# Optimization experiments

Hardware: AMD Instinct MI355X
Metric: run time of the kernel (lower is better)

## Reference

```python
import jax, jax.numpy as jnp
import numpy as np

N, F, H, R, B, L, C, E, NB = 8192, 512, 256, 16, 32, 256, 7, 262144, 30
D = F + H


def setup_inputs() -> dict:
    ks = jax.random.split(jax.random.key(0), 16)
    g = lambda k, shape, fan: jax.random.normal(k, shape, jnp.float32) / np.sqrt(fan)
    return {
        "x": jax.random.normal(ks[0], (N, F), jnp.float32),
        "edge_index": jax.random.randint(ks[1], (2, E), 0, N),
        "edge_norm": jax.random.uniform(ks[2], (E,), jnp.float32),
        "edge_type": jax.random.randint(ks[3], (E,), 0, R),
        "seq_lengths": jnp.full((B,), L, dtype=jnp.int32),
        "umask": jnp.ones((B, L), jnp.float32),
        "nodal_attn": 1,
        "avec": 0,
        "basis": g(ks[4], (NB, F, H), F),
        "comp": g(ks[5], (R, NB), NB),
        "root1": g(ks[6], (F, H), F),
        "bias1": jnp.zeros((H,), jnp.float32),
        "w_rel": g(ks[7], (H, H), H),
        "b_rel": jnp.zeros((H,), jnp.float32),
        "w_root": g(ks[8], (H, H), H),
        "w_att": g(ks[9], (D, D), D),
        "b_att": jnp.zeros((D,), jnp.float32),
        "w_lin": g(ks[10], (D, H), D),
        "b_lin": jnp.zeros((H,), jnp.float32),
        "w_fc": g(ks[11], (H, C), H),
        "b_fc": jnp.zeros((C,), jnp.float32),
    }


def reference(x, edge_index, edge_norm, edge_type, seq_lengths, umask,
              nodal_attn, avec, basis, comp, root1, bias1, w_rel, b_rel,
              w_root, w_att, b_att, w_lin, b_lin, w_fc, b_fc):
    n = x.shape[0]
    r = comp.shape[0]
    src, dst = edge_index[0], edge_index[1]
    # ---- RGCNConv (num_bases basis decomposition, mean aggregation per relation, root + bias)
    W = jnp.einsum('rb,bfh->rfh', comp, basis)             # [R,F,H]
    xw = jnp.einsum('nf,rfh->nrh', x, W)                   # [N,R,H]
    msg = xw[src, edge_type]                               # [E,H] gather per edge
    seg = dst * r + edge_type                              # per (node, relation) segment
    cnt = jax.ops.segment_sum(jnp.ones((msg.shape[0],), msg.dtype), seg, num_segments=n * r)
    msg = msg / jnp.maximum(cnt[seg], 1.0)[:, None]
    out1 = jax.ops.segment_sum(msg, dst, num_segments=n) + x @ root1 + bias1
    # ---- GraphConv (add aggregation): W_rel * sum_j h_j + b_rel + W_root * h_i
    agg2 = jax.ops.segment_sum(out1[src], dst, num_segments=n)
    out2 = agg2 @ w_rel + b_rel + out1 @ w_root
    emotions = jnp.concatenate([x, out2], axis=-1)          # [N, F+H]
    if int(nodal_attn):
        seq = np.asarray(seq_lengths)                       # static conversation lengths
        starts = np.concatenate([[0], np.cumsum(seq)[:-1]])
        lmax = int(seq.max())
        rows = [jnp.pad(jax.lax.dynamic_slice_in_dim(emotions, int(s), int(l)),
                        ((0, lmax - int(l)), (0, 0)))
                for s, l in zip(starts, seq)]
        M = jnp.stack(rows, 0).transpose(1, 0, 2)           # [L, B, D]
        mask = umask                                        # [B, L]
        # MatchingAttention 'general2', vectorized over all timesteps t
        X = M @ w_att + b_att                               # transform(x_t) for every t: [L,B,D]
        Mm = M * mask.T[:, :, None]                         # mask memory over seq dim
        scores = jnp.einsum('tbd,sbd->tbs', X, Mm) * mask[None]
        a = jax.nn.softmax(jnp.tanh(scores), axis=-1) * mask[None]
        a = a / jnp.sum(a, axis=-1, keepdims=True)
        att = jnp.einsum('tbs,sbd->tbd', a, M)              # [L,B,D]
        hidden = jax.nn.relu(att @ w_lin + b_lin)
    else:
        hidden = jax.nn.relu(emotions @ w_lin + b_lin)
    # dropout is identity in eval mode
    logits = hidden @ w_fc + b_fc
    if int(avec):
        return logits
    return jax.nn.log_softmax(logits, axis=1)  # faithful: torch uses dim=1
```

## Files before the change

### kernel.cpp

```cpp
#include <hip/hip_runtime.h>
#include <hip/hip_bf16.h>

#define NN 8192
#define FF 512
#define HH 256
#define RR 16
#define BB 32
#define LL 256
#define CC 7
#define EE 262144
#define NBASE 30
#define DD 768

constexpr int FLAG_BIAS = 1, FLAG_RELU = 4, FLAG_TANH = 8,
              FLAG_SPLITOUT = 16, FLAG_TAILOUT = 32;

typedef __attribute__((ext_vector_type(8))) short bf16x8;
typedef __attribute__((ext_vector_type(4))) float f32x4;

__global__ __launch_bounds__(256) void detect_dtype(const unsigned short* __restrict__ xs,
                                                    int* __restrict__ flag) {
  __shared__ int red[256];
  int cnt = 0;
  for (int i = threadIdx.x * 2; i < 8192; i += 512) {
    unsigned short u = xs[i];
    int e = (u >> 7) & 0xFF;
    if (e >= 0xC0) cnt++;
  }
  red[threadIdx.x] = cnt;
  __syncthreads();
  for (int s = 128; s > 0; s >>= 1) {
    if (threadIdx.x < s) red[threadIdx.x] += red[threadIdx.x + s];
    __syncthreads();
  }
  if (threadIdx.x == 0) flag[0] = (red[0] > 16) ? 1 : 0;
}

struct ConvSeg {
  const void* src;
  float* dst;
  __hip_bfloat16* hi;
  __hip_bfloat16* lo;
  int n;
  int zero;
};
struct ConvTable {
  ConvSeg seg[12];
  int count;
  long total;
};

__global__ __launch_bounds__(256) void conv_all(ConvTable t, const int* __restrict__ flag) {
  const int fp32 = flag[0];
  for (long i = (long)blockIdx.x * 256 + threadIdx.x; i < t.total;
       i += (long)gridDim.x * 256) {
    long off = i;
    int s = 0;
    while (off >= t.seg[s].n) { off -= t.seg[s].n; s++; }
    const ConvSeg& sg = t.seg[s];
    float v = 0.f;
    if (!sg.zero)
      v = fp32 ? ((const float*)sg.src)[off]
               : __bfloat162float(((const __hip_bfloat16*)sg.src)[off]);
    if (sg.dst) sg.dst[off] = v;
    if (sg.hi) {
      __hip_bfloat16 h = __float2bfloat16(v);
      sg.hi[off] = h;
      sg.lo[off] = __float2bfloat16(v - __bfloat162float(h));
    }
  }
}

__global__ __launch_bounds__(256) void split_t_b16(const void* __restrict__ src,
                                                   __hip_bfloat16* __restrict__ hi,
                                                   __hip_bfloat16* __restrict__ lo,
                                                   int R, int C, int ld, int off,
                                                   const int* __restrict__ flag) {
  const int fp32 = flag[0];
  int total = R * C;
  for (int idx = blockIdx.x * 256 + threadIdx.x; idx < total; idx += gridDim.x * 256) {
    int r = idx % R, c = idx / R;
    float v = fp32 ? ((const float*)src)[(long)r * C + c]
                   : __bfloat162float(((const __hip_bfloat16*)src)[(long)r * C + c]);
    __hip_bfloat16 h = __float2bfloat16(v);
    long d = (long)c * ld + off + r;
    hi[d] = h;
    lo[d] = __float2bfloat16(v - __bfloat162float(h));
  }
}

__global__ __launch_bounds__(256) void copy_xsplit(
    const __hip_bfloat16* __restrict__ xh, const __hip_bfloat16* __restrict__ xl,
    __hip_bfloat16* __restrict__ eh, __hip_bfloat16* __restrict__ el) {
  int idx = blockIdx.x * 256 + threadIdx.x;
  int n = idx >> 9, f = idx & 511;
  long d = (long)n * DD + f;
  eh[d] = xh[idx];
  el[d] = xl[idx];
}

__global__ __launch_bounds__(256) void transpose_b16(
    const __hip_bfloat16* __restrict__ src, __hip_bfloat16* __restrict__ dst) {
  __shared__ __hip_bfloat16 t[32][33];
  const long b = blockIdx.z;
  const int d0 = blockIdx.x * 32, s0 = blockIdx.y * 32;
  const int c = threadIdx.x & 31, rw = threadIdx.x >> 5;
  const __hip_bfloat16* sp = src + b * (LL * DD);
  __hip_bfloat16* dp = dst + b * (LL * DD);
#pragma unroll
  for (int i = 0; i < 4; ++i)
    t[rw + i * 8][c] = sp[(long)(s0 + rw + i * 8) * DD + d0 + c];
  __syncthreads();
#pragma unroll
  for (int i = 0; i < 4; ++i)
    dp[(long)(d0 + rw + i * 8) * LL + s0 + c] = t[c][rw + i * 8];
}

__global__ __launch_bounds__(256) void wt_gemm(
    const float* __restrict__ basis, const float* __restrict__ comp,
    float* __restrict__ wt_nat) {
  __shared__ float cs[RR * NBASE];
  int tid = threadIdx.x;
  for (int i = tid; i < RR * NBASE; i += 256) cs[i] = comp[i];
  __syncthreads();
  long col = (long)blockIdx.x * 256 + tid;
  float acc[RR] = {};
  for (int b = 0; b < NBASE; ++b) {
    float v = basis[(long)b * 131072 + col];
#pragma unroll
    for (int r = 0; r < RR; ++r) acc[r] += cs[r * NBASE + b] * v;
  }
#pragma unroll
  for (int r = 0; r < RR; ++r) wt_nat[(long)r * 131072 + col] = acc[r];
}

__global__ __launch_bounds__(256) void wt_transpose(
    const float* __restrict__ wt_nat,
    __hip_bfloat16* __restrict__ hi, __hip_bfloat16* __restrict__ lo) {
  __shared__ float t[32][33];
  const int r = blockIdx.z;
  const int f0 = blockIdx.y * 32, h0 = blockIdx.x * 32;
  const int c = threadIdx.x & 31, rw = threadIdx.x >> 5;
  const float* src = wt_nat + ((long)r * 512 + f0) * 256 + h0;
#pragma unroll
  for (int i = 0; i < 4; ++i)
    t[rw + i * 8][c] = src[(long)(rw + i * 8) * 256 + c];
  __syncthreads();
#pragma unroll
  for (int i = 0; i < 4; ++i) {
    int hh = rw + i * 8;
    float v = t[c][hh];
    long orow = (long)(r * 256 + h0 + hh) * 512 + f0 + c;
    __hip_bfloat16 hv = __float2bfloat16(v);
    hi[orow] = hv;
    lo[orow] = __float2bfloat16(v - __bfloat162float(hv));
  }
}

__device__ __forceinline__ void gload_lds16(const void* g, void* l) {
  __builtin_amdgcn_global_load_lds(
      (const __attribute__((address_space(1))) unsigned int*)g,
      (__attribute__((address_space(3))) unsigned int*)l, 16, 0, 0);
}

__global__ __launch_bounds__(256) void mfma_dual(
    const __hip_bfloat16* __restrict__ A, const __hip_bfloat16* __restrict__ Alo,
    const __hip_bfloat16* __restrict__ Bt, const __hip_bfloat16* __restrict__ Btlo,
    const float* __restrict__ bias, float* __restrict__ C, float* __restrict__ Ct,
    __hip_bfloat16* __restrict__ Chi, __hip_bfloat16* __restrict__ Clo,
    int K, int ldc, long sA, long sB, long sC, int flags) {
  __shared__ __hip_bfloat16 Ah[128 * 32];
  __shared__ __hip_bfloat16 Bh[128 * 32];
  __shared__ __hip_bfloat16 Al[128 * 32];
  __shared__ __hip_bfloat16 Bl[128 * 32];
  const int tid = threadIdx.x;
  const int w = tid >> 6, lane = tid & 63;
  const long z = blockIdx.z;
  {
  }
  const int nbx = gridDim.x, nby = gridDim.y;
  const int pid = blockIdx.y * nbx + blockIdx.x;
  const int G = 8 * nbx;
  const int gid = pid / G;
  const int first = gid * 8;
  const int rows = min(nby - first, 8);
  const int by = first + (pid % G) % rows;
  const int bx = (pid % G) / rows;
  const long row0 = (long)by * 128, col0 = (long)bx * 128;
  const int wm = w & 1, wn = w >> 1;
  const int srow0 = (w * 128 + lane) >> 2;
  const int srow1 = (w * 128 + 64 + lane) >> 2;
  const int kch = (lane & 3) * 8;
  const int fr = lane & 15, q = lane >> 4;
  const bool hasAlo = (Alo != nullptr);
  const __hip_bfloat16* Az = A + z * sA;
  const __hip_bfloat16* Alz = hasAlo ? (Alo + z * sA) : nullptr;
  const __hip_bfloat16* Bz = Bt + z * sB;
  const __hip_bfloat16* Blz = Btlo + z * sB;
  const long aoff0 = (row0 + srow0) * K + kch, aoff1 = (row0 + srow1) * K + kch;
  const long boff0 = (col0 + srow0) * K + kch, boff1 = (col0 + srow1) * K + kch;
  f32x4 acc[4][4] = {};
  for (int k0 = 0; k0 < K; k0 += 32) {
    gload_lds16(Az + aoff0 + k0, Ah + w * 1024);
    gload_lds16(Az + aoff1 + k0, Ah + w * 1024 + 512);
    gload_lds16(Bz + boff0 + k0, Bh + w * 1024);
    gload_lds16(Bz + boff1 + k0, Bh + w * 1024 + 512);
    gload_lds16(Blz + boff0 + k0, Bl + w * 1024);
    gload_lds16(Blz + boff1 + k0, Bl + w * 1024 + 512);
    if (hasAlo) {
      gload_lds16(Alz + aoff0 + k0, Al + w * 1024);
      gload_lds16(Alz + aoff1 + k0, Al + w * 1024 + 512);
    }
    __syncthreads();
    bf16x8 ah[4], bh[4], bl[4];
#pragma unroll
    for (int i = 0; i < 4; ++i) {
      ah[i] = *(const bf16x8*)&Ah[(wm * 64 + i * 16 + fr) * 32 + q * 8];
      bh[i] = *(const bf16x8*)&Bh[(wn * 64 + i * 16 + fr) * 32 + q * 8];
      bl[i] = *(const bf16x8*)&Bl[(wn * 64 + i * 16 + fr) * 32 + q * 8];
    }
#pragma unroll
    for (int i = 0; i < 4; ++i)
#pragma unroll
      for (int j = 0; j < 4; ++j) {
        acc[i][j] = __builtin_amdgcn_mfma_f32_16x16x32_bf16(ah[i], bh[j], acc[i][j], 0, 0, 0);
        acc[i][j] = __builtin_amdgcn_mfma_f32_16x16x32_bf16(ah[i], bl[j], acc[i][j], 0, 0, 0);
      }
    if (hasAlo) {
      bf16x8 al[4];
#pragma unroll
      for (int i = 0; i < 4; ++i)
        al[i] = *(const bf16x8*)&Al[(wm * 64 + i * 16 + fr) * 32 + q * 8];
#pragma unroll
      for (int i = 0; i < 4; ++i)
#pragma unroll
        for (int j = 0; j < 4; ++j)
          acc[i][j] = __builtin_amdgcn_mfma_f32_16x16x32_bf16(al[i], bh[j], acc[i][j], 0, 0, 0);
    }
    __syncthreads();
  }
  const int cr = (lane >> 4) * 4, cc = lane & 15;
  float* Cz = C ? (C + z * sC) : nullptr;
  __hip_bfloat16* Chz = Chi ? (Chi + z * sC) : nullptr;
  __hip_bfloat16* Clz = Clo ? (Clo + z * sC) : nullptr;
#pragma unroll
  for (int i = 0; i < 4; ++i) {
    long rbase = row0 + wm * 64 + i * 16 + cr;
#pragma unroll
    for (int j = 0; j < 4; ++j) {
      long col = col0 + wn * 64 + j * 16 + cc;
      float bv = (flags & FLAG_BIAS) ? bias[col] : 0.f;
#pragma unroll
      for (int r = 0; r < 4; ++r) {
        float v = acc[i][j][r] + bv;
        if (flags & FLAG_RELU) v = fmaxf(v, 0.f);
        if (flags & FLAG_TANH) v = tanhf(v);
        if (flags & FLAG_SPLITOUT) {
          long off = (rbase + r) * ldc + col;
          __hip_bfloat16 hv = __float2bfloat16(v);
          Chz[off] = hv;
          Clz[off] = __float2bfloat16(v - __bfloat162float(hv));
        } else if ((flags & FLAG_TAILOUT) && col >= 4096) {
          Ct[(rbase + r) * 256 + (col - 4096)] = v;
        } else {
          Cz[(rbase + r) * ldc + col] = v;
        }
      }
    }
  }
}

__global__ __launch_bounds__(256) void count_edges(
    const int* __restrict__ ei, const int* __restrict__ et, float* __restrict__ cnt) {
  int e = blockIdx.x * 256 + threadIdx.x;
  if (e < EE) atomicAdd(&cnt[ei[EE + e] * RR + et[e]], 1.0f);
}

__global__ __launch_bounds__(256) void scan_rowptr(
    const float* __restrict__ cntf, int* __restrict__ rowptr, int* __restrict__ fill) {
  __shared__ int part[256];
  int tid = threadIdx.x;
  int base = tid * 32;
  int local[32];
  int s = 0;
  for (int i = 0; i < 32; ++i) {
    local[i] = s;
    const float* c = &cntf[(base + i) * RR];
    int d = 0;
#pragma unroll
    for (int r = 0; r < RR; ++r) d += (int)c[r];
    s += d;
  }
  part[tid] = s;
  __syncthreads();
  for (int off = 1; off < 256; off <<= 1) {
    int v = (tid >= off) ? part[tid - off] : 0;
    __syncthreads();
    part[tid] += v;
    __syncthreads();
  }
  int prev = (tid == 0) ? 0 : part[tid - 1];
  for (int i = 0; i < 32; ++i) rowptr[base + i] = prev + local[i];
  if (tid == 255) rowptr[8192] = part[255];
  for (int i = tid; i < 8192; i += 256) fill[i] = 0;
}

__global__ __launch_bounds__(256) void edge_fill(
    const int* __restrict__ ei, const int* __restrict__ et,
    const int* __restrict__ rowptr, int* __restrict__ fill, int* __restrict__ eidx) {
  int e = blockIdx.x * 256 + threadIdx.x;
  if (e < EE) {
    int dst = ei[EE + e];
    int pos = rowptr[dst] + atomicAdd(&fill[dst], 1);
    eidx[pos] = ei[e] | (et[e] << 16);
  }
}

__global__ __launch_bounds__(256) void rgcn_gather(
    const int* __restrict__ rowptr, const int* __restrict__ eidx,
    const float* __restrict__ cntf, const float* __restrict__ xw,
    float* __restrict__ out1, __hip_bfloat16* __restrict__ a2o1_hi,
    __hip_bfloat16* __restrict__ a2o1_lo) {
  const int dst = blockIdx.x;
  const int h = threadIdx.x;
  __shared__ float inv[RR];
  __shared__ int se[256];
  if (h < RR) inv[h] = 1.0f / fmaxf(cntf[dst * RR + h], 1.0f);
  const int beg = rowptr[dst], end = rowptr[dst + 1];
  float acc = 0.f;
  for (int c0 = beg; c0 < end; c0 += 256) {
    int n = min(256, end - c0);
    __syncthreads();
    if (h < n) se[h] = eidx[c0 + h];
    __syncthreads();
    for (int i = 0; i < n; ++i) {
      int pk = se[i];
      int src = pk & 0xFFFF, r = pk >> 16;
      acc += xw[((long)src << 12) + (r << 8) + h] * inv[r];
    }
  }
  float tot = out1[((long)dst << 8) + h] + acc;
  out1[((long)dst << 8) + h] = tot;
  __hip_bfloat16 hv = __float2bfloat16(tot);
  long d = (long)dst * 512 + 256 + h;
  a2o1_hi[d] = hv;
  a2o1_lo[d] = __float2bfloat16(tot - __bfloat162float(hv));
}

__global__ __launch_bounds__(256) void graphconv_gather(
    const int* __restrict__ rowptr, const int* __restrict__ eidx,
    const float* __restrict__ out1, __hip_bfloat16* __restrict__ a2o1_hi,
    __hip_bfloat16* __restrict__ a2o1_lo) {
  const int dst = blockIdx.x;
  const int h = threadIdx.x;
  __shared__ int se[256];
  const int beg = rowptr[dst], end = rowptr[dst + 1];
  float acc = 0.f;
  for (int c0 = beg; c0 < end; c0 += 256) {
    int n = min(256, end - c0);
    __syncthreads();
    if (h < n) se[h] = eidx[c0 + h];
    __syncthreads();
    for (int i = 0; i < n; ++i)
      acc += out1[((long)(se[i] & 0xFFFF) << 8) + h];
  }
  __hip_bfloat16 hv = __float2bfloat16(acc);
  long d = (long)dst * 512 + h;
  a2o1_hi[d] = hv;
  a2o1_lo[d] = __float2bfloat16(acc - __bfloat162float(hv));
}

__global__ __launch_bounds__(256) void softmax256(const float* __restrict__ S,
                                                  __hip_bfloat16* __restrict__ Ab) {
  __shared__ float red[256];
  long row = blockIdx.x;
  const float* p = S + row * 256;
  int t = threadIdx.x;
  float v = p[t];
  red[t] = v;
  __syncthreads();
  for (int s = 128; s > 0; s >>= 1) {
    if (t < s) red[t] = fmaxf(red[t], red[t + s]);
    __syncthreads();
  }
  float m = red[0];
  __syncthreads();
  float e = __expf(v - m);
  red[t] = e;
  __syncthreads();
  for (int s = 128; s > 0; s >>= 1) {
    if (t < s) red[t] += red[t + s];
    __syncthreads();
  }
  Ab[row * 256 + t] = __float2bfloat16(e / red[0]);
}

__global__ __launch_bounds__(256) void logits_lsm(
    const float* __restrict__ hidden, const float* __restrict__ w_fc,
    const float* __restrict__ b_fc, void* __restrict__ out_v,
    const int* __restrict__ flag) {
  __shared__ float wf[256 * 7];
  __shared__ float lg[224];
  __shared__ float corr[7];
  int t = blockIdx.x;
  int tid = threadIdx.x;
  for (int i = tid; i < 256 * 7; i += 256) wf[i] = w_fc[i];
  __syncthreads();
  if (tid < 224) {
    int b = tid / 7, c = tid % 7;
    const float* hr = hidden + ((long)((b << 8) + t) << 8);
    float s = b_fc[c];
    for (int k = 0; k < 256; ++k) s += hr[k] * wf[k * 7 + c];
    lg[tid] = s;
  }
  __syncthreads();
  if (tid < 7) {
    float m = -1e30f;
    for (int b = 0; b < BB; ++b) m = fmaxf(m, lg[b * 7 + tid]);
    float sum = 0.f;
    for (int b = 0; b < BB; ++b) sum += __expf(lg[b * 7 + tid] - m);
    corr[tid] = m + logf(sum);
  }
  __syncthreads();
  if (tid < 224) {
    float v = lg[tid] - corr[tid % 7];
    if (flag[0]) ((float*)out_v)[t * 224 + tid] = v;
    else ((__hip_bfloat16*)out_v)[t * 224 + tid] = __float2bfloat16(v);
  }
}

extern "C" void kernel_launch(void* const* d_in, const int* in_sizes, int n_in,
                              void* d_out, int out_size, void* d_ws, size_t ws_size,
                              hipStream_t stream) {
  const int* ei = (const int*)d_in[1];
  const int* et = (const int*)d_in[3];

  float* ws = (float*)d_ws;
  int* flag = (int*)d_ws;
  float* p = ws + 16;
  auto alloc = [&](long nf) { float* r = p; p += nf; return r; };
  float* w_fc_f = alloc(1792);
  float* b_rel_f = alloc(256);
  float* biasx = alloc(4352);
  float* b_att_f = alloc(768);
  float* b_lin_f = alloc(256);
  float* b_fc_f = alloc(16);
  __hip_bfloat16* wlin_hi = (__hip_bfloat16*)alloc(98304);
  __hip_bfloat16* wlin_lo = (__hip_bfloat16*)alloc(98304);
  __hip_bfloat16* x_hi = (__hip_bfloat16*)alloc(2097152);
  __hip_bfloat16* x_lo = (__hip_bfloat16*)alloc(2097152);
  __hip_bfloat16* watt_hi = (__hip_bfloat16*)alloc(294912);
  __hip_bfloat16* watt_lo = (__hip_bfloat16*)alloc(294912);
  __hip_bfloat16* wrr_hi = (__hip_bfloat16*)alloc(65536);
  __hip_bfloat16* wrr_lo = (__hip_bfloat16*)alloc(65536);
  __hip_bfloat16* wtc_hi = (__hip_bfloat16*)alloc(1114112);
  __hip_bfloat16* wtc_lo = (__hip_bfloat16*)alloc(1114112);
  float* basis_f = alloc(3932160);
  float* comp_f = alloc(512);
  float* xw = alloc(33554432);
  float* cnt = alloc(131072);
  float* out1 = alloc(2097152);
  __hip_bfloat16* a2o1_hi = (__hip_bfloat16*)alloc(2097152);
  __hip_bfloat16* a2o1_lo = (__hip_bfloat16*)alloc(2097152);
  float* hidden = alloc(2097152);
  int* rowptr = (int*)alloc(8208);
  int* fillc = (int*)alloc(8192);
  int* eidx = (int*)alloc(262144);
  float* wt_nat = xw;
  float* em = xw;
  __hip_bfloat16* em_hi = (__hip_bfloat16*)(em + 6291456);
  __hip_bfloat16* em_lo = (__hip_bfloat16*)(em + 9437184);
  __hip_bfloat16* X_hi = (__hip_bfloat16*)(em + 12582912);
  __hip_bfloat16* X_lo = (__hip_bfloat16*)(em + 15728640);
  float* scores = em + 18874368;
  __hip_bfloat16* a_b16 = (__hip_bfloat16*)(em + 20971520);
  __hip_bfloat16* att_hi = (__hip_bfloat16*)(em + 22020096);
  __hip_bfloat16* att_lo = (__hip_bfloat16*)(em + 25165824);
  __hip_bfloat16* emT_hi = (__hip_bfloat16*)em;
  __hip_bfloat16* emT_lo = (__hip_bfloat16*)(em + 3145728);

  detect_dtype<<<1, 256, 0, stream>>>((const unsigned short*)d_in[0], flag);
  ConvTable T{};
  long tot = 0;
  int ns = 0;
  auto seg = [&](const void* s, float* d, __hip_bfloat16* hi, __hip_bfloat16* lo,
                 int n, int z) {
    T.seg[ns].src = s; T.seg[ns].dst = d; T.seg[ns].hi = hi; T.seg[ns].lo = lo;
    T.seg[ns].n = n; T.seg[ns].zero = z; ns++; tot += n;
  };
  seg(d_in[0], nullptr, x_hi, x_lo, NN * FF, 0);
  seg(d_in[8], basis_f, nullptr, nullptr, NBASE * FF * HH, 0);
  seg(d_in[9], comp_f, nullptr, nullptr, RR * NBASE, 0);
  seg(d_in[13], b_rel_f, nullptr, nullptr, HH, 0);
  seg(d_in[16], b_att_f, nullptr, nullptr, DD, 0);
  seg(d_in[18], b_lin_f, nullptr, nullptr, HH, 0);
  seg(d_in[19], w_fc_f, nullptr, nullptr, HH * CC, 0);
  seg(d_in[20], b_fc_f, nullptr, nullptr, CC, 0);
  seg(nullptr, biasx, nullptr, nullptr, 4096, 1);
  seg(d_in[11], biasx + 4096, nullptr, nullptr, HH, 0);
  T.count = ns;
  T.total = tot;
  conv_all<<<4096, 256, 0, stream>>>(T, flag);
  split_t_b16<<<2048, 256, 0, stream>>>(d_in[15], watt_hi, watt_lo, DD, DD, DD, 0, flag);
  split_t_b16<<<768, 256, 0, stream>>>(d_in[17], wlin_hi, wlin_lo, DD, HH, DD, 0, flag);
  split_t_b16<<<512, 256, 0, stream>>>(d_in[10], wtc_hi + 4096 * 512,
                                       wtc_lo + 4096 * 512, FF, HH, FF, 0, flag);
  split_t_b16<<<256, 256, 0, stream>>>(d_in[12], wrr_hi, wrr_lo, HH, HH, 512, 0, flag);
  split_t_b16<<<256, 256, 0, stream>>>(d_in[14], wrr_hi, wrr_lo, HH, HH, 512, 256, flag);

  wt_gemm<<<131072 / 256, 256, 0, stream>>>(basis_f, comp_f, wt_nat);
  wt_transpose<<<dim3(8, 16, 16), 256, 0, stream>>>(wt_nat, wtc_hi, wtc_lo);
  mfma_dual<<<dim3(34, 64, 1), 256, 0, stream>>>(
      x_hi, x_lo, wtc_hi, wtc_lo, biasx, xw, out1, nullptr, nullptr, FF, 4096,
      0, 0, 0, FLAG_BIAS | FLAG_TAILOUT);
  hipMemsetAsync(cnt, 0, 131072 * sizeof(float), stream);
  count_edges<<<EE / 256, 256, 0, stream>>>(ei, et, cnt);
  scan_rowptr<<<1, 256, 0, stream>>>(cnt, rowptr, fillc);
  edge_fill<<<EE / 256, 256, 0, stream>>>(ei, et, rowptr, fillc, eidx);
  rgcn_gather<<<NN, 256, 0, stream>>>(rowptr, eidx, cnt, xw, out1, a2o1_hi, a2o1_lo);
  graphconv_gather<<<NN, 256, 0, stream>>>(rowptr, eidx, out1, a2o1_hi, a2o1_lo);
  copy_xsplit<<<(NN * FF) / 256, 256, 0, stream>>>(x_hi, x_lo, em_hi, em_lo);
  mfma_dual<<<dim3(2, 64, 1), 256, 0, stream>>>(
      a2o1_hi, a2o1_lo, wrr_hi, wrr_lo, b_rel_f, nullptr, nullptr,
      em_hi + 512, em_lo + 512, 512, DD, 0, 0, 0, FLAG_BIAS | FLAG_SPLITOUT);
  transpose_b16<<<dim3(24, 8, 32), 256, 0, stream>>>(em_hi, emT_hi);
  transpose_b16<<<dim3(24, 8, 32), 256, 0, stream>>>(em_lo, emT_lo);
  mfma_dual<<<dim3(6, 64, 1), 256, 0, stream>>>(
      em_hi, em_lo, watt_hi, watt_lo, b_att_f, nullptr, nullptr, X_hi, X_lo, DD, DD,
      0, 0, 0, FLAG_BIAS | FLAG_SPLITOUT);
  mfma_dual<<<dim3(2, 2, BB), 256, 0, stream>>>(
      X_hi, X_lo, em_hi, em_lo, nullptr, scores, nullptr, nullptr, nullptr, DD, LL,
      (long)LL * DD, (long)LL * DD, (long)LL * LL, FLAG_TANH);
  softmax256<<<BB * LL, 256, 0, stream>>>(scores, a_b16);
  mfma_dual<<<dim3(6, 2, BB), 256, 0, stream>>>(
      a_b16, nullptr, emT_hi, emT_lo, nullptr, nullptr, nullptr, att_hi, att_lo, LL, DD,
      (long)LL * LL, (long)LL * DD, (long)LL * DD, FLAG_SPLITOUT);
  mfma_dual<<<dim3(2, 64, 1), 256, 0, stream>>>(
      att_hi, att_lo, wlin_hi, wlin_lo, b_lin_f, hidden, nullptr, nullptr, nullptr,
      DD, HH, 0, 0, 0, FLAG_BIAS | FLAG_RELU);
  logits_lsm<<<LL, 256, 0, stream>>>(hidden, w_fc_f, b_fc_f, d_out, flag);
}
```

Baseline: 697.6 us.

## Batch weight split launches, add occupancy hint, drop grouped tile swizzle in GEMM

Merges five separate transpose-and-split launches into one table-driven kernel, which cuts launch overhead. Adds a minimum-blocks-per-CU hint of 3 to the dual-bf16 MFMA GEMM. Replaces the grouped (L2-friendly) block index swizzle with a plain row/column mapping. The swizzle removal can hurt L2 reuse on the large xw GEMM, and the occupancy hint may cause register spills.

Measured after the change: 652.9 us. 1.07x faster.

```diff
diff --git a/kernel.cpp b/kernel.cpp
--- a/kernel.cpp
+++ b/kernel.cpp
@@ -71,21 +71,33 @@
   }
 }
 
-__global__ __launch_bounds__(256) void split_t_b16(const void* __restrict__ src,
-                                                   __hip_bfloat16* __restrict__ hi,
-                                                   __hip_bfloat16* __restrict__ lo,
-                                                   int R, int C, int ld, int off,
-                                                   const int* __restrict__ flag) {
+struct TSeg {
+  const void* src;
+  __hip_bfloat16* hi;
+  __hip_bfloat16* lo;
+  int R, C, ld, off;
+};
+struct TTable {
+  TSeg seg[6];
+  int count;
+  long total;
+};
+
+__global__ __launch_bounds__(256) void split_t_all(TTable t, const int* __restrict__ flag) {
   const int fp32 = flag[0];
-  int total = R * C;
-  for (int idx = blockIdx.x * 256 + threadIdx.x; idx < total; idx += gridDim.x * 256) {
-    int r = idx % R, c = idx / R;
-    float v = fp32 ? ((const float*)src)[(long)r * C + c]
-                   : __bfloat162float(((const __hip_bfloat16*)src)[(long)r * C + c]);
+  for (long i = (long)blockIdx.x * 256 + threadIdx.x; i < t.total;
+       i += (long)gridDim.x * 256) {
+    long off = i;
+    int s = 0;
+    while (off >= (long)t.seg[s].R * t.seg[s].C) { off -= (long)t.seg[s].R * t.seg[s].C; s++; }
+    const TSeg& sg = t.seg[s];
+    int r = (int)(off % sg.R), c = (int)(off / sg.R);
+    float v = fp32 ? ((const float*)sg.src)[(long)r * sg.C + c]
+                   : __bfloat162float(((const __hip_bfloat16*)sg.src)[(long)r * sg.C + c]);
     __hip_bfloat16 h = __float2bfloat16(v);
-    long d = (long)c * ld + off + r;
-    hi[d] = h;
-    lo[d] = __float2bfloat16(v - __bfloat162float(h));
+    long d = (long)c * sg.ld + sg.off + r;
+    sg.hi[d] = h;
+    sg.lo[d] = __float2bfloat16(v - __bfloat162float(h));
   }
 }
 
@@ -163,7 +175,7 @@
       (__attribute__((address_space(3))) unsigned int*)l, 16, 0, 0);
 }
 
-__global__ __launch_bounds__(256) void mfma_dual(
+__global__ __launch_bounds__(256, 3) void mfma_dual(
     const __hip_bfloat16* __restrict__ A, const __hip_bfloat16* __restrict__ Alo,
     const __hip_bfloat16* __restrict__ Bt, const __hip_bfloat16* __restrict__ Btlo,
     const float* __restrict__ bias, float* __restrict__ C, float* __restrict__ Ct,
@@ -176,17 +188,7 @@
   const int tid = threadIdx.x;
   const int w = tid >> 6, lane = tid & 63;
   const long z = blockIdx.z;
-  {
-  }
-  const int nbx = gridDim.x, nby = gridDim.y;
-  const int pid = blockIdx.y * nbx + blockIdx.x;
-  const int G = 8 * nbx;
-  const int gid = pid / G;
-  const int first = gid * 8;
-  const int rows = min(nby - first, 8);
-  const int by = first + (pid % G) % rows;
-  const int bx = (pid % G) / rows;
-  const long row0 = (long)by * 128, col0 = (long)bx * 128;
+  const long row0 = (long)blockIdx.y * 128, col0 = (long)blockIdx.x * 128;
   const int wm = w & 1, wn = w >> 1;
   const int srow0 = (w * 128 + lane) >> 2;
   const int srow1 = (w * 128 + 64 + lane) >> 2;
@@ -501,12 +503,23 @@
   T.count = ns;
   T.total = tot;
   conv_all<<<4096, 256, 0, stream>>>(T, flag);
-  split_t_b16<<<2048, 256, 0, stream>>>(d_in[15], watt_hi, watt_lo, DD, DD, DD, 0, flag);
-  split_t_b16<<<768, 256, 0, stream>>>(d_in[17], wlin_hi, wlin_lo, DD, HH, DD, 0, flag);
-  split_t_b16<<<512, 256, 0, stream>>>(d_in[10], wtc_hi + 4096 * 512,
-                                       wtc_lo + 4096 * 512, FF, HH, FF, 0, flag);
-  split_t_b16<<<256, 256, 0, stream>>>(d_in[12], wrr_hi, wrr_lo, HH, HH, 512, 0, flag);
-  split_t_b16<<<256, 256, 0, stream>>>(d_in[14], wrr_hi, wrr_lo, HH, HH, 512, 256, flag);
+  TTable TT{};
+  long ttot = 0;
+  int ts = 0;
+  auto tseg = [&](const void* s, __hip_bfloat16* hi, __hip_bfloat16* lo,
+                  int R, int C, int ld, int off) {
+    TT.seg[ts].src = s; TT.seg[ts].hi = hi; TT.seg[ts].lo = lo;
+    TT.seg[ts].R = R; TT.seg[ts].C = C; TT.seg[ts].ld = ld; TT.seg[ts].off = off;
+    ts++; ttot += (long)R * C;
+  };
+  tseg(d_in[15], watt_hi, watt_lo, DD, DD, DD, 0);
+  tseg(d_in[17], wlin_hi, wlin_lo, DD, HH, DD, 0);
+  tseg(d_in[10], wtc_hi + 4096 * 512, wtc_lo + 4096 * 512, FF, HH, FF, 0);
+  tseg(d_in[12], wrr_hi, wrr_lo, HH, HH, 512, 0);
+  tseg(d_in[14], wrr_hi, wrr_lo, HH, HH, 512, 256);
+  TT.count = ts;
+  TT.total = ttot;
+  split_t_all<<<2048, 256, 0, stream>>>(TT, flag);
 
   wt_gemm<<<131072 / 256, 256, 0, stream>>>(basis_f, comp_f, wt_nat);
   wt_transpose<<<dim3(8, 16, 16), 256, 0, stream>>>(wt_nat, wtc_hi, wtc_lo);
```
